# Performance work log

Measured on AMD Instinct MI355X. Metric: run time of the kernel, lower is better.

Reference implementation:

```python
import jax, jax.numpy as jnp
import numpy as np

B, T, M, D = 8, 256, 64, 512
H = 8
DK = D // H


def setup_inputs() -> dict:
    key = jax.random.key(0)
    ks = jax.random.split(key, 9)
    s = 1.0 / np.sqrt(D)
    return {
        "x": jax.random.normal(ks[0], (B, T, M, D), dtype=jnp.float32),
        "Wq": jax.random.normal(ks[1], (D, D), dtype=jnp.float32) * s,
        "bq": jax.random.normal(ks[2], (D,), dtype=jnp.float32) * s,
        "Wk": jax.random.normal(ks[3], (D, D), dtype=jnp.float32) * s,
        "bk": jax.random.normal(ks[4], (D,), dtype=jnp.float32) * s,
        "Wv": jax.random.normal(ks[5], (D, D), dtype=jnp.float32) * s,
        "bv": jax.random.normal(ks[6], (D,), dtype=jnp.float32) * s,
        "Wo": jax.random.normal(ks[7], (D, D), dtype=jnp.float32) * s,
        "bo": jax.random.normal(ks[8], (D,), dtype=jnp.float32) * s,
    }


def reference(x, Wq, bq, Wk, bk, Wv, bv, Wo, bo):
    # x: (B, T, M, D); attention over the M (units) axis per (B, T, head).
    scale = jnp.asarray(np.sqrt(DK), dtype=x.dtype)
    q = (x @ Wq.T + bq).reshape(B, T, M, H, DK)
    k = (x @ Wk.T + bk).reshape(B, T, M, H, DK)
    v = (x @ Wv.T + bv).reshape(B, T, M, H, DK)
    # scores: (B, T, H, M, M)
    scores = jnp.einsum("btqhd,btkhd->bthqk", q, k) / scale
    attn = jax.nn.softmax(scores, axis=-1)  # dropout is identity in eval
    out = jnp.einsum("bthqk,btkhd->btqhd", attn, v).reshape(B, T, M, D)
    return out @ Wo.T + bo
```

## Files before the change

### kernel.cpp

```cpp
#include <hip/hip_runtime.h>


typedef unsigned short u16;
typedef short s4v __attribute__((ext_vector_type(4)));
typedef short s8v __attribute__((ext_vector_type(8)));
typedef unsigned short us4 __attribute__((ext_vector_type(4)));
typedef __bf16 bf8v __attribute__((ext_vector_type(8)));
typedef float f4v __attribute__((ext_vector_type(4)));
typedef float fl4 __attribute__((ext_vector_type(4)));

#define LX 516
#define LQ 68
#define LB 36

static __device__ __forceinline__ u16 f2bf(float f) {
  union { float f; unsigned u; } v;
  v.f = f;
  unsigned r = v.u + 0x7fffu + ((v.u >> 16) & 1u);
  return (u16)(r >> 16);
}

union Frag8 { s4v h[2]; s8v v; };

static __device__ __forceinline__ s8v load_frag(const u16* p) {
  Frag8 f;
  f.h[0] = *(const s4v*)(p);
  f.h[1] = *(const s4v*)(p + 4);
  return f.v;
}

static __device__ __forceinline__ f4v mfma16(s8v a, s8v b, f4v c) {
  return __builtin_amdgcn_mfma_f32_16x16x32_bf16(
      __builtin_bit_cast(bf8v, a), __builtin_bit_cast(bf8v, b), c, 0, 0, 0);
}

__global__ __launch_bounds__(256) void pack_weights_kernel(
    const float* __restrict__ Wq, const float* __restrict__ Wk,
    const float* __restrict__ Wv, const float* __restrict__ Wo,
    u16* __restrict__ Wqkv, u16* __restrict__ Wob) {
  const int i4 = (blockIdx.x * 256 + threadIdx.x) * 4;
  fl4 a = *(const fl4*)(Wq + i4);
  fl4 b = *(const fl4*)(Wk + i4);
  fl4 c = *(const fl4*)(Wv + i4);
  fl4 d = *(const fl4*)(Wo + i4);
  us4 pa, pb, pc, pd;
#pragma unroll
  for (int t = 0; t < 4; ++t) {
    pa[t] = f2bf(a[t]); pb[t] = f2bf(b[t]);
    pc[t] = f2bf(c[t]); pd[t] = f2bf(d[t]);
  }
  *(us4*)(Wqkv + i4) = pa;
  *(us4*)(Wqkv + 262144 + i4) = pb;
  *(us4*)(Wqkv + 524288 + i4) = pc;
  *(us4*)(Wob + i4) = pd;
}

__global__ __launch_bounds__(512) void qkv_attn_kernel(
    const float* __restrict__ x, const u16* __restrict__ Wqkv,
    const float* __restrict__ bq, const float* __restrict__ bk,
    const float* __restrict__ bv, u16* __restrict__ attn) {
  __shared__ u16 x_s[64 * LX];
  __shared__ u16 qs[2][64 * LQ];
  __shared__ u16 ks_[2][64 * LQ];
  __shared__ u16 vs[2][64 * LQ];
  __shared__ u16 Ps[2][64 * LQ];

  const int bt = blockIdx.x;
  const int tid = threadIdx.x;
  const int lane = tid & 63;
  const int wave = tid >> 6;
  const int grp = wave >> 2;
  const int w = wave & 3;
  const int l15 = lane & 15;
  const int l4 = lane >> 4;

  {
    const float* xp = x + (size_t)bt * (64 * 512);
    const int c4 = (tid & 127) * 4;
    const int r0 = tid >> 7;
#pragma unroll
    for (int i = 0; i < 16; ++i) {
      const int r = r0 + i * 4;
      fl4 v = *(const fl4*)(xp + r * 512 + c4);
      us4 p;
      p[0] = f2bf(v[0]); p[1] = f2bf(v[1]);
      p[2] = f2bf(v[2]); p[3] = f2bf(v[3]);
      *(us4*)&x_s[r * LX + c4] = p;
    }
  }
  __syncthreads();

  const f4v fzero = {0.f, 0.f, 0.f, 0.f};

  for (int hi = 0; hi < 4; ++hi) {
    const int h = grp * 4 + hi;
    const int ncol = h * 64 + 16 * w + l15;
    const float bqv = bq[ncol];
    const float bkv = bk[ncol];
    const float bvv = bv[ncol];
    const u16* WqP = Wqkv + (size_t)ncol * 512 + l4 * 8;
    const u16* WkP = Wqkv + (size_t)(512 + ncol) * 512 + l4 * 8;
    const u16* WvP = Wqkv + (size_t)(1024 + ncol) * 512 + l4 * 8;

    f4v aq[4], ak[4], av[4];
#pragma unroll
    for (int i = 0; i < 4; ++i) { aq[i] = fzero; ak[i] = fzero; av[i] = fzero; }

#pragma unroll
    for (int kk = 0; kk < 16; ++kk) {
      const int ko = kk * 32 + l4 * 8;
      const s8v bq8 = *(const s8v*)(WqP + kk * 32);
      const s8v bk8 = *(const s8v*)(WkP + kk * 32);
      const s8v bv8 = *(const s8v*)(WvP + kk * 32);
      const s8v a0 = load_frag(&x_s[(0 + l15) * LX + ko]);
      const s8v a1 = load_frag(&x_s[(16 + l15) * LX + ko]);
      const s8v a2 = load_frag(&x_s[(32 + l15) * LX + ko]);
      const s8v a3 = load_frag(&x_s[(48 + l15) * LX + ko]);
      aq[0] = mfma16(a0, bq8, aq[0]); aq[1] = mfma16(a1, bq8, aq[1]);
      aq[2] = mfma16(a2, bq8, aq[2]); aq[3] = mfma16(a3, bq8, aq[3]);
      ak[0] = mfma16(a0, bk8, ak[0]); ak[1] = mfma16(a1, bk8, ak[1]);
      ak[2] = mfma16(a2, bk8, ak[2]); ak[3] = mfma16(a3, bk8, ak[3]);
      av[0] = mfma16(a0, bv8, av[0]); av[1] = mfma16(a1, bv8, av[1]);
      av[2] = mfma16(a2, bv8, av[2]); av[3] = mfma16(a3, bv8, av[3]);
    }

    const int nl = 16 * w + l15;
#pragma unroll
    for (int i = 0; i < 4; ++i) {
#pragma unroll
      for (int r = 0; r < 4; ++r) {
        const int m = 16 * i + 4 * l4 + r;
        qs[grp][m * LQ + nl] = f2bf((aq[i][r] + bqv) * 0.125f);
        ks_[grp][m * LQ + nl] = f2bf(ak[i][r] + bkv);
        vs[grp][nl * LQ + m] = f2bf(av[i][r] + bvv);
      }
    }
    __syncthreads();

    f4v s[4];
#pragma unroll
    for (int j = 0; j < 4; ++j) s[j] = fzero;
#pragma unroll
    for (int kc = 0; kc < 2; ++kc) {
      const s8v af = load_frag(&qs[grp][(16 * w + l15) * LQ + kc * 32 + l4 * 8]);
#pragma unroll
      for (int j = 0; j < 4; ++j) {
        const s8v bf = load_frag(&ks_[grp][(16 * j + l15) * LQ + kc * 32 + l4 * 8]);
        s[j] = mfma16(af, bf, s[j]);
      }
    }
#pragma unroll
    for (int r = 0; r < 4; ++r) {
      float mx = fmaxf(fmaxf(s[0][r], s[1][r]), fmaxf(s[2][r], s[3][r]));
      mx = fmaxf(mx, __shfl_xor(mx, 1));
      mx = fmaxf(mx, __shfl_xor(mx, 2));
      mx = fmaxf(mx, __shfl_xor(mx, 4));
      mx = fmaxf(mx, __shfl_xor(mx, 8));
      float e0 = __expf(s[0][r] - mx);
      float e1 = __expf(s[1][r] - mx);
      float e2 = __expf(s[2][r] - mx);
      float e3 = __expf(s[3][r] - mx);
      float sm = e0 + e1 + e2 + e3;
      sm += __shfl_xor(sm, 1);
      sm += __shfl_xor(sm, 2);
      sm += __shfl_xor(sm, 4);
      sm += __shfl_xor(sm, 8);
      const float inv = __builtin_amdgcn_rcpf(sm);
      s[0][r] = e0 * inv; s[1][r] = e1 * inv;
      s[2][r] = e2 * inv; s[3][r] = e3 * inv;
    }
#pragma unroll
    for (int j = 0; j < 4; ++j)
#pragma unroll
      for (int r = 0; r < 4; ++r)
        Ps[grp][(16 * w + 4 * l4 + r) * LQ + 16 * j + l15] = f2bf(s[j][r]);
    __syncthreads();

    f4v o[4];
#pragma unroll
    for (int j = 0; j < 4; ++j) o[j] = fzero;
#pragma unroll
    for (int kc = 0; kc < 2; ++kc) {
      const s8v af = load_frag(&Ps[grp][(16 * w + l15) * LQ + kc * 32 + l4 * 8]);
#pragma unroll
      for (int j = 0; j < 4; ++j) {
        const s8v bf = load_frag(&vs[grp][(16 * j + l15) * LQ + kc * 32 + l4 * 8]);
        o[j] = mfma16(af, bf, o[j]);
      }
    }
    u16* ap = attn + (size_t)(bt * 64) * 512 + h * 64;
#pragma unroll
    for (int j = 0; j < 4; ++j)
#pragma unroll
      for (int r = 0; r < 4; ++r)
        ap[(size_t)(16 * w + 4 * l4 + r) * 512 + 16 * j + l15] = f2bf(o[j][r]);
    __syncthreads();
  }
}

__global__ __launch_bounds__(256) void out_proj_kernel(
    const u16* __restrict__ attn, const u16* __restrict__ Wob,
    const float* __restrict__ bo, float* __restrict__ out) {
  __shared__ u16 As[128 * LB];
  __shared__ u16 Bs[128 * LB];
  const int m0 = blockIdx.x * 128;
  const int n0 = blockIdx.y * 128;
  const int tid = threadIdx.x;
  const int lane = tid & 63;
  const int wave = tid >> 6;
  const int wy = wave >> 1;
  const int wx = wave & 1;
  const int l15 = lane & 15;
  const int l4 = lane >> 4;

  const f4v fzero = {0.f, 0.f, 0.f, 0.f};
  f4v acc[4][4];
#pragma unroll
  for (int i = 0; i < 4; ++i)
#pragma unroll
    for (int j = 0; j < 4; ++j) acc[i][j] = fzero;

  const int row0 = tid >> 2, cc0 = (tid & 3) * 8;
  const int c1 = tid + 256;
  const int row1 = c1 >> 2, cc1 = (c1 & 3) * 8;

  for (int k0 = 0; k0 < 512; k0 += 32) {
    __syncthreads();
    {
      Frag8 ga0, gb0, ga1, gb1;
      ga0.v = *(const s8v*)(attn + (size_t)(m0 + row0) * 512 + k0 + cc0);
      gb0.v = *(const s8v*)(Wob + (size_t)(n0 + row0) * 512 + k0 + cc0);
      ga1.v = *(const s8v*)(attn + (size_t)(m0 + row1) * 512 + k0 + cc1);
      gb1.v = *(const s8v*)(Wob + (size_t)(n0 + row1) * 512 + k0 + cc1);
      *(s4v*)&As[row0 * LB + cc0] = ga0.h[0];
      *(s4v*)&As[row0 * LB + cc0 + 4] = ga0.h[1];
      *(s4v*)&Bs[row0 * LB + cc0] = gb0.h[0];
      *(s4v*)&Bs[row0 * LB + cc0 + 4] = gb0.h[1];
      *(s4v*)&As[row1 * LB + cc1] = ga1.h[0];
      *(s4v*)&As[row1 * LB + cc1 + 4] = ga1.h[1];
      *(s4v*)&Bs[row1 * LB + cc1] = gb1.h[0];
      *(s4v*)&Bs[row1 * LB + cc1 + 4] = gb1.h[1];
    }
    __syncthreads();
    s8v a[4], b[4];
#pragma unroll
    for (int i = 0; i < 4; ++i)
      a[i] = load_frag(&As[(wy * 64 + 16 * i + l15) * LB + l4 * 8]);
#pragma unroll
    for (int j = 0; j < 4; ++j)
      b[j] = load_frag(&Bs[(wx * 64 + 16 * j + l15) * LB + l4 * 8]);
#pragma unroll
    for (int i = 0; i < 4; ++i)
#pragma unroll
      for (int j = 0; j < 4; ++j)
        acc[i][j] = mfma16(a[i], b[j], acc[i][j]);
  }
#pragma unroll
  for (int j = 0; j < 4; ++j) {
    const int col = n0 + wx * 64 + 16 * j + l15;
    const float bb = bo[col];
#pragma unroll
    for (int i = 0; i < 4; ++i) {
#pragma unroll
      for (int r = 0; r < 4; ++r) {
        const int row = m0 + wy * 64 + 16 * i + 4 * l4 + r;
        out[(size_t)row * 512 + col] = acc[i][j][r] + bb;
      }
    }
  }
}

extern "C" void kernel_launch(void* const* d_in, const int* in_sizes, int n_in,
                              void* d_out, int out_size, void* d_ws, size_t ws_size,
                              hipStream_t stream) {
  const float* x  = (const float*)d_in[0];
  const float* Wq = (const float*)d_in[1];
  const float* bq = (const float*)d_in[2];
  const float* Wk = (const float*)d_in[3];
  const float* bk = (const float*)d_in[4];
  const float* Wv = (const float*)d_in[5];
  const float* bv = (const float*)d_in[6];
  const float* Wo = (const float*)d_in[7];
  const float* bo = (const float*)d_in[8];
  float* out = (float*)d_out;

  u16* Wqkv = (u16*)d_ws;
  u16* Wob  = Wqkv + 3 * 512 * 512;
  u16* attn = Wob + 512 * 512;

  pack_weights_kernel<<<256, 256, 0, stream>>>(Wq, Wk, Wv, Wo, Wqkv, Wob);
  qkv_attn_kernel<<<2048, 512, 0, stream>>>(x, Wqkv, bq, bk, bv, attn);
  out_proj_kernel<<<dim3(1024, 4), 256, 0, stream>>>(attn, Wob, bo, out);
}
```

Measured before the change: 1.009 ms.

## Split QKV-attention blocks per head group, pre-cast x, use direct global-to-LDS loads

Converts x to bf16 in a separate kernel, writing into the output buffer as scratch. The QKV+attention kernel now runs two 256-thread blocks per (b,t), one per head group, with no large x tile in LDS. It reads x fragments straight from global memory (mostly from cache), which lowers LDS use and should allow more resident blocks. The out-projection kernel stages its tiles with global_load_lds instead of register round-trips, at the cost of an unpadded LDS layout that may cause bank conflicts.

Result: slower. 1.847 ms (+83.1%).

```diff
diff --git a/kernel.cpp b/kernel.cpp
--- a/kernel.cpp
+++ b/kernel.cpp
@@ -5,13 +5,12 @@
 typedef short s4v __attribute__((ext_vector_type(4)));
 typedef short s8v __attribute__((ext_vector_type(8)));
 typedef unsigned short us4 __attribute__((ext_vector_type(4)));
+typedef unsigned short us8 __attribute__((ext_vector_type(8)));
 typedef __bf16 bf8v __attribute__((ext_vector_type(8)));
 typedef float f4v __attribute__((ext_vector_type(4)));
 typedef float fl4 __attribute__((ext_vector_type(4)));
 
-#define LX 516
 #define LQ 68
-#define LB 36
 
 static __device__ __forceinline__ u16 f2bf(float f) {
   union { float f; unsigned u; } v;
@@ -32,6 +31,12 @@
 static __device__ __forceinline__ f4v mfma16(s8v a, s8v b, f4v c) {
   return __builtin_amdgcn_mfma_f32_16x16x32_bf16(
       __builtin_bit_cast(bf8v, a), __builtin_bit_cast(bf8v, b), c, 0, 0, 0);
+}
+
+static __device__ __forceinline__ void gload_lds16(const u16* g, u16* lds) {
+  __builtin_amdgcn_global_load_lds(
+      (const __attribute__((address_space(1))) void*)g,
+      (__attribute__((address_space(3))) void*)lds, 16, 0, 0);
 }
 
 __global__ __launch_bounds__(256) void pack_weights_kernel(
@@ -55,41 +60,39 @@
   *(us4*)(Wob + i4) = pd;
 }
 
-__global__ __launch_bounds__(512) void qkv_attn_kernel(
-    const float* __restrict__ x, const u16* __restrict__ Wqkv,
+__global__ __launch_bounds__(256) void xcast_kernel(const float* __restrict__ x,
+                                                    u16* __restrict__ xb) {
+  const int t = blockIdx.x * 256 + threadIdx.x;
+#pragma unroll
+  for (int i = 0; i < 16; ++i) {
+    const size_t c8 = ((size_t)i * 524288 + (size_t)t) * 8;
+    fl4 v0 = *(const fl4*)(x + c8);
+    fl4 v1 = *(const fl4*)(x + c8 + 4);
+    us8 p;
+#pragma unroll
+    for (int j = 0; j < 4; ++j) { p[j] = f2bf(v0[j]); p[4 + j] = f2bf(v1[j]); }
+    *(us8*)(xb + c8) = p;
+  }
+}
+
+__global__ __launch_bounds__(256, 4) void qkv_attn_kernel(
+    const u16* __restrict__ xb, const u16* __restrict__ Wqkv,
     const float* __restrict__ bq, const float* __restrict__ bk,
     const float* __restrict__ bv, u16* __restrict__ attn) {
-  __shared__ u16 x_s[64 * LX];
-  __shared__ u16 qs[2][64 * LQ];
-  __shared__ u16 ks_[2][64 * LQ];
-  __shared__ u16 vs[2][64 * LQ];
-  __shared__ u16 Ps[2][64 * LQ];
-
-  const int bt = blockIdx.x;
+  __shared__ u16 qs[64 * LQ];
+  __shared__ u16 ks_[64 * LQ];
+  __shared__ u16 vs[64 * LQ];
+  __shared__ u16 Ps[64 * LQ];
+
+  const int bt = blockIdx.x >> 1;
+  const int grp = blockIdx.x & 1;
   const int tid = threadIdx.x;
   const int lane = tid & 63;
-  const int wave = tid >> 6;
-  const int grp = wave >> 2;
-  const int w = wave & 3;
+  const int w = tid >> 6;
   const int l15 = lane & 15;
   const int l4 = lane >> 4;
 
-  {
-    const float* xp = x + (size_t)bt * (64 * 512);
-    const int c4 = (tid & 127) * 4;
-    const int r0 = tid >> 7;
-#pragma unroll
-    for (int i = 0; i < 16; ++i) {
-      const int r = r0 + i * 4;
-      fl4 v = *(const fl4*)(xp + r * 512 + c4);
-      us4 p;
-      p[0] = f2bf(v[0]); p[1] = f2bf(v[1]);
-      p[2] = f2bf(v[2]); p[3] = f2bf(v[3]);
-      *(us4*)&x_s[r * LX + c4] = p;
-    }
-  }
-  __syncthreads();
-
+  const u16* xw = xb + (size_t)bt * (64 * 512) + (size_t)l15 * 512 + l4 * 8;
   const f4v fzero = {0.f, 0.f, 0.f, 0.f};
 
   for (int hi = 0; hi < 4; ++hi) {
@@ -99,8 +102,6 @@
     const float bkv = bk[ncol];
     const float bvv = bv[ncol];
     const u16* WqP = Wqkv + (size_t)ncol * 512 + l4 * 8;
-    const u16* WkP = Wqkv + (size_t)(512 + ncol) * 512 + l4 * 8;
-    const u16* WvP = Wqkv + (size_t)(1024 + ncol) * 512 + l4 * 8;
 
     f4v aq[4], ak[4], av[4];
 #pragma unroll
@@ -108,14 +109,13 @@
 
 #pragma unroll
     for (int kk = 0; kk < 16; ++kk) {
-      const int ko = kk * 32 + l4 * 8;
       const s8v bq8 = *(const s8v*)(WqP + kk * 32);
-      const s8v bk8 = *(const s8v*)(WkP + kk * 32);
-      const s8v bv8 = *(const s8v*)(WvP + kk * 32);
-      const s8v a0 = load_frag(&x_s[(0 + l15) * LX + ko]);
-      const s8v a1 = load_frag(&x_s[(16 + l15) * LX + ko]);
-      const s8v a2 = load_frag(&x_s[(32 + l15) * LX + ko]);
-      const s8v a3 = load_frag(&x_s[(48 + l15) * LX + ko]);
+      const s8v bk8 = *(const s8v*)(WqP + 262144 + kk * 32);
+      const s8v bv8 = *(const s8v*)(WqP + 524288 + kk * 32);
+      const s8v a0 = *(const s8v*)(xw + kk * 32);
+      const s8v a1 = *(const s8v*)(xw + 16 * 512 + kk * 32);
+      const s8v a2 = *(const s8v*)(xw + 32 * 512 + kk * 32);
+      const s8v a3 = *(const s8v*)(xw + 48 * 512 + kk * 32);
       aq[0] = mfma16(a0, bq8, aq[0]); aq[1] = mfma16(a1, bq8, aq[1]);
       aq[2] = mfma16(a2, bq8, aq[2]); aq[3] = mfma16(a3, bq8, aq[3]);
       ak[0] = mfma16(a0, bk8, ak[0]); ak[1] = mfma16(a1, bk8, ak[1]);
@@ -130,9 +130,9 @@
 #pragma unroll
       for (int r = 0; r < 4; ++r) {
         const int m = 16 * i + 4 * l4 + r;
-        qs[grp][m * LQ + nl] = f2bf((aq[i][r] + bqv) * 0.125f);
-        ks_[grp][m * LQ + nl] = f2bf(ak[i][r] + bkv);
-        vs[grp][nl * LQ + m] = f2bf(av[i][r] + bvv);
+        qs[m * LQ + nl] = f2bf((aq[i][r] + bqv) * 0.125f);
+        ks_[m * LQ + nl] = f2bf(ak[i][r] + bkv);
+        vs[nl * LQ + m] = f2bf(av[i][r] + bvv);
       }
     }
     __syncthreads();
@@ -142,10 +142,10 @@
     for (int j = 0; j < 4; ++j) s[j] = fzero;
 #pragma unroll
     for (int kc = 0; kc < 2; ++kc) {
-      const s8v af = load_frag(&qs[grp][(16 * w + l15) * LQ + kc * 32 + l4 * 8]);
+      const s8v af = load_frag(&qs[(16 * w + l15) * LQ + kc * 32 + l4 * 8]);
 #pragma unroll
       for (int j = 0; j < 4; ++j) {
-        const s8v bf = load_frag(&ks_[grp][(16 * j + l15) * LQ + kc * 32 + l4 * 8]);
+        const s8v bf = load_frag(&ks_[(16 * j + l15) * LQ + kc * 32 + l4 * 8]);
         s[j] = mfma16(af, bf, s[j]);
       }
     }
@@ -173,7 +173,7 @@
     for (int j = 0; j < 4; ++j)
 #pragma unroll
       for (int r = 0; r < 4; ++r)
-        Ps[grp][(16 * w + 4 * l4 + r) * LQ + 16 * j + l15] = f2bf(s[j][r]);
+        Ps[(16 * w + 4 * l4 + r) * LQ + 16 * j + l15] = f2bf(s[j][r]);
     __syncthreads();
 
     f4v o[4];
@@ -181,10 +181,10 @@
     for (int j = 0; j < 4; ++j) o[j] = fzero;
 #pragma unroll
     for (int kc = 0; kc < 2; ++kc) {
-      const s8v af = load_frag(&Ps[grp][(16 * w + l15) * LQ + kc * 32 + l4 * 8]);
+      const s8v af = load_frag(&Ps[(16 * w + l15) * LQ + kc * 32 + l4 * 8]);
 #pragma unroll
       for (int j = 0; j < 4; ++j) {
-        const s8v bf = load_frag(&vs[grp][(16 * j + l15) * LQ + kc * 32 + l4 * 8]);
+        const s8v bf = load_frag(&vs[(16 * j + l15) * LQ + kc * 32 + l4 * 8]);
         o[j] = mfma16(af, bf, o[j]);
       }
     }
@@ -201,8 +201,8 @@
 __global__ __launch_bounds__(256) void out_proj_kernel(
     const u16* __restrict__ attn, const u16* __restrict__ Wob,
     const float* __restrict__ bo, float* __restrict__ out) {
-  __shared__ u16 As[128 * LB];
-  __shared__ u16 Bs[128 * LB];
+  __shared__ __align__(16) u16 As[128 * 32];
+  __shared__ __align__(16) u16 Bs[128 * 32];
   const int m0 = blockIdx.x * 128;
   const int n0 = blockIdx.y * 128;
   const int tid = threadIdx.x;
@@ -213,6 +213,16 @@
   const int l15 = lane & 15;
   const int l4 = lane >> 4;
 
+  const int r0 = wave * 32;
+  const int lrow = lane >> 2;
+  const int lcol = (lane & 3) * 8;
+  const u16* Ag = attn + (size_t)(m0 + r0 + lrow) * 512 + lcol;
+  const u16* Bg = Wob + (size_t)(n0 + r0 + lrow) * 512 + lcol;
+  u16* As0 = &As[r0 * 32];
+  u16* As1 = &As[(r0 + 16) * 32];
+  u16* Bs0 = &Bs[r0 * 32];
+  u16* Bs1 = &Bs[(r0 + 16) * 32];
+
   const f4v fzero = {0.f, 0.f, 0.f, 0.f};
   f4v acc[4][4];
 #pragma unroll
@@ -220,35 +230,20 @@
 #pragma unroll
     for (int j = 0; j < 4; ++j) acc[i][j] = fzero;
 
-  const int row0 = tid >> 2, cc0 = (tid & 3) * 8;
-  const int c1 = tid + 256;
-  const int row1 = c1 >> 2, cc1 = (c1 & 3) * 8;
-
   for (int k0 = 0; k0 < 512; k0 += 32) {
     __syncthreads();
-    {
-      Frag8 ga0, gb0, ga1, gb1;
-      ga0.v = *(const s8v*)(attn + (size_t)(m0 + row0) * 512 + k0 + cc0);
-      gb0.v = *(const s8v*)(Wob + (size_t)(n0 + row0) * 512 + k0 + cc0);
-      ga1.v = *(const s8v*)(attn + (size_t)(m0 + row1) * 512 + k0 + cc1);
-      gb1.v = *(const s8v*)(Wob + (size_t)(n0 + row1) * 512 + k0 + cc1);
-      *(s4v*)&As[row0 * LB + cc0] = ga0.h[0];
-      *(s4v*)&As[row0 * LB + cc0 + 4] = ga0.h[1];
-      *(s4v*)&Bs[row0 * LB + cc0] = gb0.h[0];
-      *(s4v*)&Bs[row0 * LB + cc0 + 4] = gb0.h[1];
-      *(s4v*)&As[row1 * LB + cc1] = ga1.h[0];
-      *(s4v*)&As[row1 * LB + cc1 + 4] = ga1.h[1];
-      *(s4v*)&Bs[row1 * LB + cc1] = gb1.h[0];
-      *(s4v*)&Bs[row1 * LB + cc1 + 4] = gb1.h[1];
-    }
+    gload_lds16(Ag + k0, As0);
+    gload_lds16(Ag + 16 * 512 + k0, As1);
+    gload_lds16(Bg + k0, Bs0);
+    gload_lds16(Bg + 16 * 512 + k0, Bs1);
     __syncthreads();
     s8v a[4], b[4];
 #pragma unroll
     for (int i = 0; i < 4; ++i)
-      a[i] = load_frag(&As[(wy * 64 + 16 * i + l15) * LB + l4 * 8]);
+      a[i] = *(const s8v*)&As[(wy * 64 + 16 * i + l15) * 32 + l4 * 8];
 #pragma unroll
     for (int j = 0; j < 4; ++j)
-      b[j] = load_frag(&Bs[(wx * 64 + 16 * j + l15) * LB + l4 * 8]);
+      b[j] = *(const s8v*)&Bs[(wx * 64 + 16 * j + l15) * 32 + l4 * 8];
 #pragma unroll
     for (int i = 0; i < 4; ++i)
 #pragma unroll
@@ -287,8 +282,10 @@
   u16* Wqkv = (u16*)d_ws;
   u16* Wob  = Wqkv + 3 * 512 * 512;
   u16* attn = Wob + 512 * 512;
+  u16* xb = (u16*)d_out;
 
   pack_weights_kernel<<<256, 256, 0, stream>>>(Wq, Wk, Wv, Wo, Wqkv, Wob);
-  qkv_attn_kernel<<<2048, 512, 0, stream>>>(x, Wqkv, bq, bk, bv, attn);
+  xcast_kernel<<<2048, 256, 0, stream>>>(x, xb);
+  qkv_attn_kernel<<<4096, 256, 0, stream>>>(xb, Wqkv, bq, bk, bv, attn);
   out_proj_kernel<<<dim3(1024, 4), 256, 0, stream>>>(attn, Wob, bo, out);
 }
```
